# Kernel optimization log

Measured on AMD Instinct MI355X. Metric: run time of the kernel, lower is better.

The kernel has to match this reference:

```python
import jax, jax.numpy as jnp
import numpy as np

B, T, N, D, H = 16, 128, 64, 256, 512

def _xavier(key, shape):
    fan_in, fan_out = shape[0], shape[1]
    limit = float(np.sqrt(6.0 / (fan_in + fan_out)))
    return jax.random.uniform(key, shape, jnp.float32, -limit, limit)

def setup_inputs() -> dict:
    key = jax.random.key(0)
    ks = jax.random.split(key, 12)
    inp = {
        'x1': jax.random.normal(ks[0], (B, T, N, D), jnp.float32),
        'x2': jax.random.normal(ks[1], (B, T, N, D), jnp.float32),
        'Wq1': _xavier(ks[2], (D, H)),
        'Wk1': _xavier(ks[3], (D, H)),
        'Wv1': _xavier(ks[4], (D, H)),
        'Wq2': _xavier(ks[5], (D, H)),
        'Wk2': _xavier(ks[6], (D, H)),
        'Wv2': _xavier(ks[7], (D, H)),
        'W1': _xavier(ks[8], (2 * H, H)),
        'b1': jnp.zeros((H,), jnp.float32),
        'W2': _xavier(ks[9], (H, H)),
        'b2': jnp.zeros((H,), jnp.float32),
    }
    return inp

def reference(x1, x2, Wq1, Wk1, Wv1, Wq2, Wk2, Wv2, W1, b1, W2, b2):
    scale = x1.shape[-1] ** (-0.5)  # scales by in_dim, as in the original
    q1 = jnp.einsum('btnd,dh->btnh', x1, Wq1) * scale
    k1 = jnp.einsum('btnd,dh->btnh', x1, Wk1)
    v1 = jnp.einsum('btnd,dh->btnh', x1, Wv1)
    q2 = jnp.einsum('btnd,dh->btnh', x2, Wq2) * scale
    k2 = jnp.einsum('btnd,dh->btnh', x2, Wk2)
    v2 = jnp.einsum('btnd,dh->btnh', x2, Wv2)
    # cross attention 1: q1 attends over k2, aggregates v1 (faithful to source)
    s1 = jnp.einsum('btnh,btmh->btnm', q1, k2)
    a1 = jnp.einsum('btnm,btmh->btnh', jax.nn.softmax(s1, axis=-1), v1)
    # cross attention 2: q2 attends over k1, aggregates v2
    s2 = jnp.einsum('btnh,btmh->btnm', q2, k1)
    a2 = jnp.einsum('btnm,btmh->btnh', jax.nn.softmax(s2, axis=-1), v2)
    x = jnp.concatenate([a1, a2], axis=-1)  # [B,T,N,2H]
    h = jax.nn.relu(jnp.einsum('btnf,fh->btnh', x, W1) + b1)
    return jnp.einsum('btnh,hk->btnk', h, W2) + b2
```

## Files before the change

### kernel.cpp

```cpp
#include <hip/hip_runtime.h>
#include <stdint.h>

#define NB 64
#define DD 256
#define HH 512
#define NGROUP 2048

typedef __attribute__((ext_vector_type(8))) _Float16 half8;
typedef __attribute__((ext_vector_type(4))) _Float16 half4;
typedef __attribute__((ext_vector_type(4))) float f32x4;

__device__ __forceinline__ half8 ld8(const _Float16* p) {
    return *reinterpret_cast<const half8*>(p);
}

__device__ __forceinline__ int fragidx(int R, int K, int NKS) {
    return (((R >> 4) * NKS + (K >> 5)) * 64 + (((K >> 3) & 3) * 16 + (R & 15))) * 8 + (K & 7);
}

__global__ void prep_all(const float* __restrict__ Wq1, const float* __restrict__ Wk1,
                         const float* __restrict__ Wv1, const float* __restrict__ Wq2,
                         const float* __restrict__ Wk2, const float* __restrict__ Wv2,
                         const float* __restrict__ W1, const float* __restrict__ W2,
                         _Float16* __restrict__ Gf1, _Float16* __restrict__ Gf2,
                         _Float16* __restrict__ UTf, _Float16* __restrict__ W2Tf,
                         float scale) {
    const int b = blockIdx.x, t = threadIdx.x;
    if (b < 512) {
        const float* A = (b < 256) ? Wq1 : Wq2;
        const float* Bm = (b < 256) ? Wk2 : Wk1;
        _Float16* G = (b < 256) ? Gf1 : Gf2;
        const int d = b & 255, e = t;
        const float4* qa = reinterpret_cast<const float4*>(A + d * HH);
        const float4* ka = reinterpret_cast<const float4*>(Bm + e * HH);
        float s = 0.f;
        #pragma unroll 8
        for (int j = 0; j < HH / 4; ++j) {
            float4 a = qa[j], bb = ka[j];
            s += a.x * bb.x + a.y * bb.y + a.z * bb.z + a.w * bb.w;
        }
        G[fragidx(d, e, 8)] = (_Float16)(s * scale);
    } else if (b < 1536) {
        const int half = (b - 512) >> 9;
        const int o = (b - 512) & 511;
        const float* Wv = half ? Wv2 : Wv1;
        const float* W1p = W1 + half * HH * HH;
        const int d = t;
        const float4* va = reinterpret_cast<const float4*>(Wv + d * HH);
        float s = 0.f;
        #pragma unroll 4
        for (int j4 = 0; j4 < HH / 4; ++j4) {
            float4 a = va[j4];
            const int j = j4 * 4;
            s += a.x * W1p[(j + 0) * HH + o];
            s += a.y * W1p[(j + 1) * HH + o];
            s += a.z * W1p[(j + 2) * HH + o];
            s += a.w * W1p[(j + 3) * HH + o];
        }
        UTf[fragidx(o, half * 256 + d, 16)] = (_Float16)s;
    } else {
        __shared__ float tile[32][33];
        const int bi = b - 1536;
        const int bk = (bi & 15) * 32;
        const int bh = (bi >> 4) * 32;
        const int tx = t & 31, ty = t >> 5;
        #pragma unroll
        for (int i = 0; i < 32; i += 8)
            tile[ty + i][tx] = W2[(bh + ty + i) * HH + bk + tx];
        __syncthreads();
        #pragma unroll
        for (int i = 0; i < 32; i += 8) {
            const int R = bk + ty + i;
            const int K = bh + tx;
            W2Tf[fragidx(R, K, 16)] = (_Float16)tile[tx][ty + i];
        }
    }
}

#define ABASE 65536
#define PBASE 131072

__device__ __forceinline__ int axX(int side, int row, int ec) {
    return side * 32768 + row * 512 +
           ((2 * ec) ^ ((row & 7) << 4) ^ (((row >> 3) & 1) << 7));
}
__device__ __forceinline__ int axA(int side, int row, int ec) {
    return ABASE + side * 32768 + row * 512 +
           ((2 * ec) ^ ((row & 7) << 4) ^ (((row >> 3) & 1) << 7));
}
__device__ __forceinline__ int axXT(int side, int row, int ec) {
    return ABASE + side * 32768 + row * 128 + ((2 * ec) ^ ((row & 7) << 4));
}
__device__ __forceinline__ int axH(int row, int ec) {
    return ABASE + row * 1024 +
           ((2 * ec) ^ ((row & 7) << 4) ^ (((row >> 3) & 1) << 7));
}
__device__ __forceinline__ int axP(int side, int row, int ec) {
    return PBASE + side * 8192 + row * 128 + ((2 * ec) ^ ((row & 7) << 4));
}

__global__ __launch_bounds__(1024, 4)
void fused_kernel(const float* __restrict__ x1g, const float* __restrict__ x2g,
                  const _Float16* __restrict__ Gf1, const _Float16* __restrict__ Gf2,
                  const _Float16* __restrict__ UTf, const _Float16* __restrict__ W2Tf,
                  const float* __restrict__ b1, const float* __restrict__ b2,
                  float* __restrict__ out) {
    __shared__ __align__(16) char lds[147456];

    const int tid = threadIdx.x;
    const int lane = tid & 63;
    const int w = tid >> 6;
    const int c = lane & 15;
    const int kg = lane >> 4;
    const int s = w >> 3;
    const int ws = w & 7;
    const size_t g = blockIdx.x;
    const f32x4 z = {0.f, 0.f, 0.f, 0.f};

    {
        const float* xs0 = x1g + g * (NB * DD);
        const float* xs1 = x2g + g * (NB * DD);
        #pragma unroll
        for (int it = 0; it < 4; ++it) {
            const int row = 4 * w + it;
            float4 a = reinterpret_cast<const float4*>(xs0 + row * DD)[lane];
            float4 b = reinterpret_cast<const float4*>(xs1 + row * DD)[lane];
            half4 ha, hb;
            ha[0] = (_Float16)a.x; ha[1] = (_Float16)a.y; ha[2] = (_Float16)a.z; ha[3] = (_Float16)a.w;
            hb[0] = (_Float16)b.x; hb[1] = (_Float16)b.y; hb[2] = (_Float16)b.z; hb[3] = (_Float16)b.w;
            *reinterpret_cast<half4*>(lds + axX(0, row, 4 * lane)) = ha;
            *reinterpret_cast<half4*>(lds + axX(1, row, 4 * lane)) = hb;
        }
    }
    __syncthreads();

    {
        const _Float16* Gsel = s ? Gf2 : Gf1;
        const int xo = 1 - s;
        f32x4 acc[4][2];
        #pragma unroll
        for (int i = 0; i < 4; ++i) { acc[i][0] = z; acc[i][1] = z; }
        #pragma unroll
        for (int ks = 0; ks < 8; ++ks) {
            half8 af[4];
            #pragma unroll
            for (int i = 0; i < 4; ++i)
                af[i] = *reinterpret_cast<const half8*>(lds + axX(xo, 16 * i + c, 32 * ks + 8 * kg));
            #pragma unroll
            for (int ct = 0; ct < 2; ++ct) {
                half8 bf = ld8(Gsel + (((2 * ws + ct) * 8 + ks) * 64 + lane) * 8);
                #pragma unroll
                for (int i = 0; i < 4; ++i)
                    acc[i][ct] = __builtin_amdgcn_mfma_f32_16x16x32_f16(af[i], bf, acc[i][ct], 0, 0, 0);
            }
        }
        #pragma unroll
        for (int i = 0; i < 4; ++i)
            #pragma unroll
            for (int ct = 0; ct < 2; ++ct)
                #pragma unroll
                for (int r = 0; r < 4; ++r)
                    *reinterpret_cast<_Float16*>(lds + axA(s, 16 * i + 4 * kg + r, 32 * ws + 16 * ct + c)) = (_Float16)acc[i][ct][r];
    }
    __syncthreads();

    if ((w & 4) == 0) {
        const int wa = w & 3;
        f32x4 Sacc[4] = {z, z, z, z};
        #pragma unroll
        for (int ks = 0; ks < 8; ++ks) {
            half8 af = *reinterpret_cast<const half8*>(lds + axX(s, 16 * wa + c, 32 * ks + 8 * kg));
            #pragma unroll
            for (int j = 0; j < 4; ++j) {
                half8 bfr = *reinterpret_cast<const half8*>(lds + axA(s, 16 * j + c, 32 * ks + 8 * kg));
                Sacc[j] = __builtin_amdgcn_mfma_f32_16x16x32_f16(af, bfr, Sacc[j], 0, 0, 0);
            }
        }
        #pragma unroll
        for (int r = 0; r < 4; ++r) {
            float m0 = fmaxf(fmaxf(Sacc[0][r], Sacc[1][r]), fmaxf(Sacc[2][r], Sacc[3][r]));
            m0 = fmaxf(m0, __shfl_xor(m0, 1));
            m0 = fmaxf(m0, __shfl_xor(m0, 2));
            m0 = fmaxf(m0, __shfl_xor(m0, 4));
            m0 = fmaxf(m0, __shfl_xor(m0, 8));
            float e0 = __expf(Sacc[0][r] - m0);
            float e1 = __expf(Sacc[1][r] - m0);
            float e2 = __expf(Sacc[2][r] - m0);
            float e3 = __expf(Sacc[3][r] - m0);
            float s0 = e0 + e1 + e2 + e3;
            s0 += __shfl_xor(s0, 1);
            s0 += __shfl_xor(s0, 2);
            s0 += __shfl_xor(s0, 4);
            s0 += __shfl_xor(s0, 8);
            const float inv = 1.f / s0;
            const int row = 16 * wa + 4 * kg + r;
            *reinterpret_cast<_Float16*>(lds + axP(s, row, 16 * 0 + c)) = (_Float16)(e0 * inv);
            *reinterpret_cast<_Float16*>(lds + axP(s, row, 16 * 1 + c)) = (_Float16)(e1 * inv);
            *reinterpret_cast<_Float16*>(lds + axP(s, row, 16 * 2 + c)) = (_Float16)(e2 * inv);
            *reinterpret_cast<_Float16*>(lds + axP(s, row, 16 * 3 + c)) = (_Float16)(e3 * inv);
        }
    }
    __syncthreads();

    {
        #pragma unroll
        for (int jj = 0; jj < 4; ++jj) {
            half8 v = *reinterpret_cast<const half8*>(lds + axX(s, lane, 32 * ws + 8 * jj));
            #pragma unroll
            for (int e = 0; e < 8; ++e)
                *reinterpret_cast<_Float16*>(lds + axXT(s, 32 * ws + 8 * jj + e, lane)) = v[e];
        }
    }
    __syncthreads();

    {
        half8 paf[4][2];
        #pragma unroll
        for (int i = 0; i < 4; ++i)
            #pragma unroll
            for (int ksp = 0; ksp < 2; ++ksp)
                paf[i][ksp] = *reinterpret_cast<const half8*>(lds + axP(s, 16 * i + c, 32 * ksp + 8 * kg));
        #pragma unroll
        for (int dt = 0; dt < 2; ++dt) {
            half8 bfr0 = *reinterpret_cast<const half8*>(lds + axXT(s, 32 * ws + 16 * dt + c, 8 * kg));
            half8 bfr1 = *reinterpret_cast<const half8*>(lds + axXT(s, 32 * ws + 16 * dt + c, 32 + 8 * kg));
            #pragma unroll
            for (int i = 0; i < 4; ++i) {
                f32x4 acc = z;
                acc = __builtin_amdgcn_mfma_f32_16x16x32_f16(paf[i][0], bfr0, acc, 0, 0, 0);
                acc = __builtin_amdgcn_mfma_f32_16x16x32_f16(paf[i][1], bfr1, acc, 0, 0, 0);
                #pragma unroll
                for (int r = 0; r < 4; ++r)
                    *reinterpret_cast<_Float16*>(lds + axX(s, 16 * i + 4 * kg + r, 32 * ws + 16 * dt + c)) = (_Float16)acc[r];
            }
        }
    }
    __syncthreads();

    {
        f32x4 acc[4][2];
        #pragma unroll
        for (int i = 0; i < 4; ++i) { acc[i][0] = z; acc[i][1] = z; }
        #pragma unroll
        for (int ks = 0; ks < 16; ++ks) {
            const int side = ks >> 3, kk = ks & 7;
            half8 af[4];
            #pragma unroll
            for (int i = 0; i < 4; ++i)
                af[i] = *reinterpret_cast<const half8*>(lds + axX(side, 16 * i + c, 32 * kk + 8 * kg));
            #pragma unroll
            for (int ct = 0; ct < 2; ++ct) {
                half8 bf = ld8(UTf + (((2 * w + ct) * 16 + ks) * 64 + lane) * 8);
                #pragma unroll
                for (int i = 0; i < 4; ++i)
                    acc[i][ct] = __builtin_amdgcn_mfma_f32_16x16x32_f16(af[i], bf, acc[i][ct], 0, 0, 0);
            }
        }
        #pragma unroll
        for (int ct = 0; ct < 2; ++ct) {
            const float bb = b1[32 * w + 16 * ct + c];
            #pragma unroll
            for (int i = 0; i < 4; ++i)
                #pragma unroll
                for (int r = 0; r < 4; ++r)
                    *reinterpret_cast<_Float16*>(lds + axH(16 * i + 4 * kg + r, 32 * w + 16 * ct + c)) =
                        (_Float16)fmaxf(acc[i][ct][r] + bb, 0.f);
        }
    }
    __syncthreads();

    {
        f32x4 oacc[2][4];
        #pragma unroll
        for (int i = 0; i < 2; ++i)
            #pragma unroll
            for (int nj = 0; nj < 4; ++nj) oacc[i][nj] = z;
        #pragma unroll
        for (int ks = 0; ks < 16; ++ks) {
            half8 bfr2[4];
            #pragma unroll
            for (int nj = 0; nj < 4; ++nj)
                bfr2[nj] = *reinterpret_cast<const half8*>(lds + axH(16 * nj + c, 32 * ks + 8 * kg));
            #pragma unroll
            for (int i = 0; i < 2; ++i) {
                half8 af2 = ld8(W2Tf + (((2 * w + i) * 16 + ks) * 64 + lane) * 8);
                #pragma unroll
                for (int nj = 0; nj < 4; ++nj)
                    oacc[i][nj] = __builtin_amdgcn_mfma_f32_16x16x32_f16(af2, bfr2[nj], oacc[i][nj], 0, 0, 0);
            }
        }
        float* og = out + g * (size_t)(NB * HH);
        #pragma unroll
        for (int nj = 0; nj < 4; ++nj) {
            float* orow = og + (size_t)(16 * nj + c) * HH;
            #pragma unroll
            for (int i = 0; i < 2; ++i) {
                const int ocol0 = 32 * w + 16 * i + 4 * kg;
                const float4 b2v = *reinterpret_cast<const float4*>(b2 + ocol0);
                float4 res;
                res.x = oacc[i][nj][0] + b2v.x;
                res.y = oacc[i][nj][1] + b2v.y;
                res.z = oacc[i][nj][2] + b2v.z;
                res.w = oacc[i][nj][3] + b2v.w;
                *reinterpret_cast<float4*>(orow + ocol0) = res;
            }
        }
    }
}


extern "C" void kernel_launch(void* const* d_in, const int* in_sizes, int n_in,
                              void* d_out, int out_size, void* d_ws, size_t ws_size,
                              hipStream_t stream) {
    (void)in_sizes; (void)n_in; (void)out_size; (void)ws_size;
    const float* x1  = (const float*)d_in[0];
    const float* x2  = (const float*)d_in[1];
    const float* Wq1 = (const float*)d_in[2];
    const float* Wk1 = (const float*)d_in[3];
    const float* Wv1 = (const float*)d_in[4];
    const float* Wq2 = (const float*)d_in[5];
    const float* Wk2 = (const float*)d_in[6];
    const float* Wv2 = (const float*)d_in[7];
    const float* W1  = (const float*)d_in[8];
    const float* b1  = (const float*)d_in[9];
    const float* W2  = (const float*)d_in[10];
    const float* b2  = (const float*)d_in[11];
    float* out = (float*)d_out;

    char* ws = (char*)d_ws;
    _Float16* Gf1  = (_Float16*)(ws + 0);
    _Float16* Gf2  = (_Float16*)(ws + 131072);
    _Float16* UTf  = (_Float16*)(ws + 262144);
    _Float16* W2Tf = (_Float16*)(ws + 786432);

    const float scale = 0.0625f;

    prep_all<<<1792, 256, 0, stream>>>(Wq1, Wk1, Wv1, Wq2, Wk2, Wv2, W1, W2,
                                       Gf1, Gf2, UTf, W2Tf, scale);
    fused_kernel<<<NGROUP, 1024, 0, stream>>>(x1, x2, Gf1, Gf2, UTf, W2Tf, b1, b2, out);
}
```

Before: 437.9 us.

## Make fused kernel persistent over 8 groups with register-prefetched next inputs

The grid drops from 2048 blocks to 256 persistent blocks, each looping over 8 consecutive (b,t) groups. During the MLP stages the next group's x1/x2 tiles are loaded into registers, then converted to fp16 and written to LDS after the W2 GEMM, so global input latency overlaps with compute. The cost is more register pressure from the prefetch buffers and less parallelism: 256 blocks of 1024 threads with 144KB LDS each, which may leave some of the 256 CUs idle or unevenly loaded.

```diff
diff --git a/kernel.cpp b/kernel.cpp
--- a/kernel.cpp
+++ b/kernel.cpp
@@ -5,6 +5,7 @@
 #define DD 256
 #define HH 512
 #define NGROUP 2048
+#define NPERS 256
 
 typedef __attribute__((ext_vector_type(8))) _Float16 half8;
 typedef __attribute__((ext_vector_type(4))) _Float16 half4;
@@ -114,12 +115,12 @@
     const int kg = lane >> 4;
     const int s = w >> 3;
     const int ws = w & 7;
-    const size_t g = blockIdx.x;
     const f32x4 z = {0.f, 0.f, 0.f, 0.f};
 
     {
-        const float* xs0 = x1g + g * (NB * DD);
-        const float* xs1 = x2g + g * (NB * DD);
+        const size_t g0 = (size_t)blockIdx.x * 8;
+        const float* xs0 = x1g + g0 * (NB * DD);
+        const float* xs1 = x2g + g0 * (NB * DD);
         #pragma unroll
         for (int it = 0; it < 4; ++it) {
             const int row = 4 * w + it;
@@ -134,177 +135,209 @@
     }
     __syncthreads();
 
-    {
-        const _Float16* Gsel = s ? Gf2 : Gf1;
-        const int xo = 1 - s;
-        f32x4 acc[4][2];
-        #pragma unroll
-        for (int i = 0; i < 4; ++i) { acc[i][0] = z; acc[i][1] = z; }
-        #pragma unroll
-        for (int ks = 0; ks < 8; ++ks) {
-            half8 af[4];
+    #pragma unroll 1
+    for (int itg = 0; itg < 8; ++itg) {
+        const size_t g = (size_t)blockIdx.x * 8 + itg;
+
+        {
+            const _Float16* Gsel = s ? Gf2 : Gf1;
+            const int xo = 1 - s;
+            f32x4 acc[4][2];
+            #pragma unroll
+            for (int i = 0; i < 4; ++i) { acc[i][0] = z; acc[i][1] = z; }
+            #pragma unroll
+            for (int ks = 0; ks < 8; ++ks) {
+                half8 af[4];
+                #pragma unroll
+                for (int i = 0; i < 4; ++i)
+                    af[i] = *reinterpret_cast<const half8*>(lds + axX(xo, 16 * i + c, 32 * ks + 8 * kg));
+                #pragma unroll
+                for (int ct = 0; ct < 2; ++ct) {
+                    half8 bf = ld8(Gsel + (((2 * ws + ct) * 8 + ks) * 64 + lane) * 8);
+                    #pragma unroll
+                    for (int i = 0; i < 4; ++i)
+                        acc[i][ct] = __builtin_amdgcn_mfma_f32_16x16x32_f16(af[i], bf, acc[i][ct], 0, 0, 0);
+                }
+            }
             #pragma unroll
             for (int i = 0; i < 4; ++i)
-                af[i] = *reinterpret_cast<const half8*>(lds + axX(xo, 16 * i + c, 32 * ks + 8 * kg));
+                #pragma unroll
+                for (int ct = 0; ct < 2; ++ct)
+                    #pragma unroll
+                    for (int r = 0; r < 4; ++r)
+                        *reinterpret_cast<_Float16*>(lds + axA(s, 16 * i + 4 * kg + r, 32 * ws + 16 * ct + c)) = (_Float16)acc[i][ct][r];
+        }
+        __syncthreads();
+
+        if ((w & 4) == 0) {
+            const int wa = w & 3;
+            f32x4 Sacc[4] = {z, z, z, z};
+            #pragma unroll
+            for (int ks = 0; ks < 8; ++ks) {
+                half8 af = *reinterpret_cast<const half8*>(lds + axX(s, 16 * wa + c, 32 * ks + 8 * kg));
+                #pragma unroll
+                for (int j = 0; j < 4; ++j) {
+                    half8 bfr = *reinterpret_cast<const half8*>(lds + axA(s, 16 * j + c, 32 * ks + 8 * kg));
+                    Sacc[j] = __builtin_amdgcn_mfma_f32_16x16x32_f16(af, bfr, Sacc[j], 0, 0, 0);
+                }
+            }
+            #pragma unroll
+            for (int r = 0; r < 4; ++r) {
+                float m0 = fmaxf(fmaxf(Sacc[0][r], Sacc[1][r]), fmaxf(Sacc[2][r], Sacc[3][r]));
+                m0 = fmaxf(m0, __shfl_xor(m0, 1));
+                m0 = fmaxf(m0, __shfl_xor(m0, 2));
+                m0 = fmaxf(m0, __shfl_xor(m0, 4));
+                m0 = fmaxf(m0, __shfl_xor(m0, 8));
+                float e0 = __expf(Sacc[0][r] - m0);
+                float e1 = __expf(Sacc[1][r] - m0);
+                float e2 = __expf(Sacc[2][r] - m0);
+                float e3 = __expf(Sacc[3][r] - m0);
+                float s0 = e0 + e1 + e2 + e3;
+                s0 += __shfl_xor(s0, 1);
+                s0 += __shfl_xor(s0, 2);
+                s0 += __shfl_xor(s0, 4);
+                s0 += __shfl_xor(s0, 8);
+                const float inv = 1.f / s0;
+                const int row = 16 * wa + 4 * kg + r;
+                *reinterpret_cast<_Float16*>(lds + axP(s, row, 16 * 0 + c)) = (_Float16)(e0 * inv);
+                *reinterpret_cast<_Float16*>(lds + axP(s, row, 16 * 1 + c)) = (_Float16)(e1 * inv);
+                *reinterpret_cast<_Float16*>(lds + axP(s, row, 16 * 2 + c)) = (_Float16)(e2 * inv);
+                *reinterpret_cast<_Float16*>(lds + axP(s, row, 16 * 3 + c)) = (_Float16)(e3 * inv);
+            }
+        }
+        __syncthreads();
+
+        {
+            #pragma unroll
+            for (int jj = 0; jj < 4; ++jj) {
+                half8 v = *reinterpret_cast<const half8*>(lds + axX(s, lane, 32 * ws + 8 * jj));
+                #pragma unroll
+                for (int e = 0; e < 8; ++e)
+                    *reinterpret_cast<_Float16*>(lds + axXT(s, 32 * ws + 8 * jj + e, lane)) = v[e];
+            }
+        }
+        __syncthreads();
+
+        {
+            half8 paf[4][2];
+            #pragma unroll
+            for (int i = 0; i < 4; ++i)
+                #pragma unroll
+                for (int ksp = 0; ksp < 2; ++ksp)
+                    paf[i][ksp] = *reinterpret_cast<const half8*>(lds + axP(s, 16 * i + c, 32 * ksp + 8 * kg));
+            #pragma unroll
+            for (int dt = 0; dt < 2; ++dt) {
+                half8 bfr0 = *reinterpret_cast<const half8*>(lds + axXT(s, 32 * ws + 16 * dt + c, 8 * kg));
+                half8 bfr1 = *reinterpret_cast<const half8*>(lds + axXT(s, 32 * ws + 16 * dt + c, 32 + 8 * kg));
+                #pragma unroll
+                for (int i = 0; i < 4; ++i) {
+                    f32x4 acc = z;
+                    acc = __builtin_amdgcn_mfma_f32_16x16x32_f16(paf[i][0], bfr0, acc, 0, 0, 0);
+                    acc = __builtin_amdgcn_mfma_f32_16x16x32_f16(paf[i][1], bfr1, acc, 0, 0, 0);
+                    #pragma unroll
+                    for (int r = 0; r < 4; ++r)
+                        *reinterpret_cast<_Float16*>(lds + axX(s, 16 * i + 4 * kg + r, 32 * ws + 16 * dt + c)) = (_Float16)acc[r];
+                }
+            }
+        }
+        __syncthreads();
+
+        float4 nx0[4], nx1[4];
+        const size_t gn = (size_t)blockIdx.x * 8 + ((itg < 7) ? (itg + 1) : itg);
+        {
+            const float* xs0 = x1g + gn * (NB * DD);
+            const float* xs1 = x2g + gn * (NB * DD);
+            #pragma unroll
+            for (int it = 0; it < 4; ++it) {
+                const int row = 4 * w + it;
+                nx0[it] = reinterpret_cast<const float4*>(xs0 + row * DD)[lane];
+                nx1[it] = reinterpret_cast<const float4*>(xs1 + row * DD)[lane];
+            }
+        }
+
+        {
+            f32x4 acc[4][2];
+            #pragma unroll
+            for (int i = 0; i < 4; ++i) { acc[i][0] = z; acc[i][1] = z; }
+            #pragma unroll
+            for (int ks = 0; ks < 16; ++ks) {
+                const int side = ks >> 3, kk = ks & 7;
+                half8 af[4];
+                #pragma unroll
+                for (int i = 0; i < 4; ++i)
+                    af[i] = *reinterpret_cast<const half8*>(lds + axX(side, 16 * i + c, 32 * kk + 8 * kg));
+                #pragma unroll
+                for (int ct = 0; ct < 2; ++ct) {
+                    half8 bf = ld8(UTf + (((2 * w + ct) * 16 + ks) * 64 + lane) * 8);
+                    #pragma unroll
+                    for (int i = 0; i < 4; ++i)
+                        acc[i][ct] = __builtin_amdgcn_mfma_f32_16x16x32_f16(af[i], bf, acc[i][ct], 0, 0, 0);
+                }
+            }
             #pragma unroll
             for (int ct = 0; ct < 2; ++ct) {
-                half8 bf = ld8(Gsel + (((2 * ws + ct) * 8 + ks) * 64 + lane) * 8);
+                const float bb = b1[32 * w + 16 * ct + c];
                 #pragma unroll
                 for (int i = 0; i < 4; ++i)
-                    acc[i][ct] = __builtin_amdgcn_mfma_f32_16x16x32_f16(af[i], bf, acc[i][ct], 0, 0, 0);
-            }
-        }
-        #pragma unroll
-        for (int i = 0; i < 4; ++i)
-            #pragma unroll
-            for (int ct = 0; ct < 2; ++ct)
-                #pragma unroll
-                for (int r = 0; r < 4; ++r)
-                    *reinterpret_cast<_Float16*>(lds + axA(s, 16 * i + 4 * kg + r, 32 * ws + 16 * ct + c)) = (_Float16)acc[i][ct][r];
-    }
-    __syncthreads();
-
-    if ((w & 4) == 0) {
-        const int wa = w & 3;
-        f32x4 Sacc[4] = {z, z, z, z};
-        #pragma unroll
-        for (int ks = 0; ks < 8; ++ks) {
-            half8 af = *reinterpret_cast<const half8*>(lds + axX(s, 16 * wa + c, 32 * ks + 8 * kg));
-            #pragma unroll
-            for (int j = 0; j < 4; ++j) {
-                half8 bfr = *reinterpret_cast<const half8*>(lds + axA(s, 16 * j + c, 32 * ks + 8 * kg));
-                Sacc[j] = __builtin_amdgcn_mfma_f32_16x16x32_f16(af, bfr, Sacc[j], 0, 0, 0);
-            }
-        }
-        #pragma unroll
-        for (int r = 0; r < 4; ++r) {
-            float m0 = fmaxf(fmaxf(Sacc[0][r], Sacc[1][r]), fmaxf(Sacc[2][r], Sacc[3][r]));
-            m0 = fmaxf(m0, __shfl_xor(m0, 1));
-            m0 = fmaxf(m0, __shfl_xor(m0, 2));
-            m0 = fmaxf(m0, __shfl_xor(m0, 4));
-            m0 = fmaxf(m0, __shfl_xor(m0, 8));
-            float e0 = __expf(Sacc[0][r] - m0);
-            float e1 = __expf(Sacc[1][r] - m0);
-            float e2 = __expf(Sacc[2][r] - m0);
-            float e3 = __expf(Sacc[3][r] - m0);
-            float s0 = e0 + e1 + e2 + e3;
-            s0 += __shfl_xor(s0, 1);
-            s0 += __shfl_xor(s0, 2);
-            s0 += __shfl_xor(s0, 4);
-            s0 += __shfl_xor(s0, 8);
-            const float inv = 1.f / s0;
-            const int row = 16 * wa + 4 * kg + r;
-            *reinterpret_cast<_Float16*>(lds + axP(s, row, 16 * 0 + c)) = (_Float16)(e0 * inv);
-            *reinterpret_cast<_Float16*>(lds + axP(s, row, 16 * 1 + c)) = (_Float16)(e1 * inv);
-            *reinterpret_cast<_Float16*>(lds + axP(s, row, 16 * 2 + c)) = (_Float16)(e2 * inv);
-            *reinterpret_cast<_Float16*>(lds + axP(s, row, 16 * 3 + c)) = (_Float16)(e3 * inv);
-        }
-    }
-    __syncthreads();
-
-    {
-        #pragma unroll
-        for (int jj = 0; jj < 4; ++jj) {
-            half8 v = *reinterpret_cast<const half8*>(lds + axX(s, lane, 32 * ws + 8 * jj));
-            #pragma unroll
-            for (int e = 0; e < 8; ++e)
-                *reinterpret_cast<_Float16*>(lds + axXT(s, 32 * ws + 8 * jj + e, lane)) = v[e];
-        }
-    }
-    __syncthreads();
-
-    {
-        half8 paf[4][2];
-        #pragma unroll
-        for (int i = 0; i < 4; ++i)
-            #pragma unroll
-            for (int ksp = 0; ksp < 2; ++ksp)
-                paf[i][ksp] = *reinterpret_cast<const half8*>(lds + axP(s, 16 * i + c, 32 * ksp + 8 * kg));
-        #pragma unroll
-        for (int dt = 0; dt < 2; ++dt) {
-            half8 bfr0 = *reinterpret_cast<const half8*>(lds + axXT(s, 32 * ws + 16 * dt + c, 8 * kg));
-            half8 bfr1 = *reinterpret_cast<const half8*>(lds + axXT(s, 32 * ws + 16 * dt + c, 32 + 8 * kg));
-            #pragma unroll
-            for (int i = 0; i < 4; ++i) {
-                f32x4 acc = z;
-                acc = __builtin_amdgcn_mfma_f32_16x16x32_f16(paf[i][0], bfr0, acc, 0, 0, 0);
-                acc = __builtin_amdgcn_mfma_f32_16x16x32_f16(paf[i][1], bfr1, acc, 0, 0, 0);
-                #pragma unroll
-                for (int r = 0; r < 4; ++r)
-                    *reinterpret_cast<_Float16*>(lds + axX(s, 16 * i + 4 * kg + r, 32 * ws + 16 * dt + c)) = (_Float16)acc[r];
-            }
-        }
-    }
-    __syncthreads();
-
-    {
-        f32x4 acc[4][2];
-        #pragma unroll
-        for (int i = 0; i < 4; ++i) { acc[i][0] = z; acc[i][1] = z; }
-        #pragma unroll
-        for (int ks = 0; ks < 16; ++ks) {
-            const int side = ks >> 3, kk = ks & 7;
-            half8 af[4];
-            #pragma unroll
-            for (int i = 0; i < 4; ++i)
-                af[i] = *reinterpret_cast<const half8*>(lds + axX(side, 16 * i + c, 32 * kk + 8 * kg));
-            #pragma unroll
-            for (int ct = 0; ct < 2; ++ct) {
-                half8 bf = ld8(UTf + (((2 * w + ct) * 16 + ks) * 64 + lane) * 8);
-                #pragma unroll
-                for (int i = 0; i < 4; ++i)
-                    acc[i][ct] = __builtin_amdgcn_mfma_f32_16x16x32_f16(af[i], bf, acc[i][ct], 0, 0, 0);
-            }
-        }
-        #pragma unroll
-        for (int ct = 0; ct < 2; ++ct) {
-            const float bb = b1[32 * w + 16 * ct + c];
-            #pragma unroll
-            for (int i = 0; i < 4; ++i)
-                #pragma unroll
-                for (int r = 0; r < 4; ++r)
-                    *reinterpret_cast<_Float16*>(lds + axH(16 * i + 4 * kg + r, 32 * w + 16 * ct + c)) =
-                        (_Float16)fmaxf(acc[i][ct][r] + bb, 0.f);
-        }
-    }
-    __syncthreads();
-
-    {
-        f32x4 oacc[2][4];
-        #pragma unroll
-        for (int i = 0; i < 2; ++i)
-            #pragma unroll
-            for (int nj = 0; nj < 4; ++nj) oacc[i][nj] = z;
-        #pragma unroll
-        for (int ks = 0; ks < 16; ++ks) {
-            half8 bfr2[4];
-            #pragma unroll
-            for (int nj = 0; nj < 4; ++nj)
-                bfr2[nj] = *reinterpret_cast<const half8*>(lds + axH(16 * nj + c, 32 * ks + 8 * kg));
-            #pragma unroll
-            for (int i = 0; i < 2; ++i) {
-                half8 af2 = ld8(W2Tf + (((2 * w + i) * 16 + ks) * 64 + lane) * 8);
+                    #pragma unroll
+                    for (int r = 0; r < 4; ++r)
+                        *reinterpret_cast<_Float16*>(lds + axH(16 * i + 4 * kg + r, 32 * w + 16 * ct + c)) =
+                            (_Float16)fmaxf(acc[i][ct][r] + bb, 0.f);
+            }
+        }
+        __syncthreads();
+
+        {
+            f32x4 oacc[2][4];
+            #pragma unroll
+            for (int i = 0; i < 2; ++i)
+                #pragma unroll
+                for (int nj = 0; nj < 4; ++nj) oacc[i][nj] = z;
+            #pragma unroll
+            for (int ks = 0; ks < 16; ++ks) {
+                half8 bfr2[4];
                 #pragma unroll
                 for (int nj = 0; nj < 4; ++nj)
-                    oacc[i][nj] = __builtin_amdgcn_mfma_f32_16x16x32_f16(af2, bfr2[nj], oacc[i][nj], 0, 0, 0);
-            }
-        }
-        float* og = out + g * (size_t)(NB * HH);
-        #pragma unroll
-        for (int nj = 0; nj < 4; ++nj) {
-            float* orow = og + (size_t)(16 * nj + c) * HH;
-            #pragma unroll
-            for (int i = 0; i < 2; ++i) {
-                const int ocol0 = 32 * w + 16 * i + 4 * kg;
-                const float4 b2v = *reinterpret_cast<const float4*>(b2 + ocol0);
-                float4 res;
-                res.x = oacc[i][nj][0] + b2v.x;
-                res.y = oacc[i][nj][1] + b2v.y;
-                res.z = oacc[i][nj][2] + b2v.z;
-                res.w = oacc[i][nj][3] + b2v.w;
-                *reinterpret_cast<float4*>(orow + ocol0) = res;
-            }
-        }
+                    bfr2[nj] = *reinterpret_cast<const half8*>(lds + axH(16 * nj + c, 32 * ks + 8 * kg));
+                #pragma unroll
+                for (int i = 0; i < 2; ++i) {
+                    half8 af2 = ld8(W2Tf + (((2 * w + i) * 16 + ks) * 64 + lane) * 8);
+                    #pragma unroll
+                    for (int nj = 0; nj < 4; ++nj)
+                        oacc[i][nj] = __builtin_amdgcn_mfma_f32_16x16x32_f16(af2, bfr2[nj], oacc[i][nj], 0, 0, 0);
+                }
+            }
+            if (itg < 7) {
+                #pragma unroll
+                for (int it = 0; it < 4; ++it) {
+                    const int row = 4 * w + it;
+                    half4 ha, hb;
+                    ha[0] = (_Float16)nx0[it].x; ha[1] = (_Float16)nx0[it].y;
+                    ha[2] = (_Float16)nx0[it].z; ha[3] = (_Float16)nx0[it].w;
+                    hb[0] = (_Float16)nx1[it].x; hb[1] = (_Float16)nx1[it].y;
+                    hb[2] = (_Float16)nx1[it].z; hb[3] = (_Float16)nx1[it].w;
+                    *reinterpret_cast<half4*>(lds + axX(0, row, 4 * lane)) = ha;
+                    *reinterpret_cast<half4*>(lds + axX(1, row, 4 * lane)) = hb;
+                }
+            }
+            float* og = out + g * (size_t)(NB * HH);
+            #pragma unroll
+            for (int nj = 0; nj < 4; ++nj) {
+                float* orow = og + (size_t)(16 * nj + c) * HH;
+                #pragma unroll
+                for (int i = 0; i < 2; ++i) {
+                    const int ocol0 = 32 * w + 16 * i + 4 * kg;
+                    const float4 b2v = *reinterpret_cast<const float4*>(b2 + ocol0);
+                    float4 res;
+                    res.x = oacc[i][nj][0] + b2v.x;
+                    res.y = oacc[i][nj][1] + b2v.y;
+                    res.z = oacc[i][nj][2] + b2v.z;
+                    res.w = oacc[i][nj][3] + b2v.w;
+                    *reinterpret_cast<float4*>(orow + ocol0) = res;
+                }
+            }
+        }
+        __syncthreads();
     }
 }
 
@@ -337,5 +370,5 @@
 
     prep_all<<<1792, 256, 0, stream>>>(Wq1, Wk1, Wv1, Wq2, Wk2, Wv2, W1, W2,
                                        Gf1, Gf2, UTf, W2Tf, scale);
-    fused_kernel<<<NGROUP, 1024, 0, stream>>>(x1, x2, Gf1, Gf2, UTf, W2Tf, b1, b2, out);
-}
+    fused_kernel<<<NPERS, 1024, 0, stream>>>(x1, x2, Gf1, Gf2, UTf, W2Tf, b1, b2, out);
+}
```

After: 1.719 ms. +292.6%, slower.
